# Optimization experiments

Hardware: AMD Instinct MI355X
Metric: run time of the kernel (lower is better)

Reference implementation:

```python
import jax, jax.numpy as jnp
import numpy as np

# Dimensions (Llama-3-8B-style GQA with paged KV cache)
B, S, HID = 1, 1024, 4096
H, HKV, D = 32, 8, 128
G = H // HKV
BLK = 16            # tokens per KV block
NB = 256            # blocks in storage
CB = 192            # context blocks attended (3072 tokens)
PAST = 2048         # tokens already cached before this step
NL = 2              # layers in kv_ptr
L = CB * BLK


def rotate_half(x):
    x1, x2 = x[..., : x.shape[-1] // 2], x[..., x.shape[-1] // 2:]
    return jnp.concatenate([-x2, x1], axis=-1)


def setup_inputs() -> dict:
    key = jax.random.key(0)
    ks = jax.random.split(key, 8)
    hidden_states = jax.random.normal(ks[0], (B, S, HID), jnp.float32)
    kv_ptr = jax.random.normal(ks[1], (NL, 2, NB, HKV, BLK, D), jnp.float32)
    Wq = 0.02 * jax.random.normal(ks[2], (H * D, HID), jnp.float32)
    Wk = 0.02 * jax.random.normal(ks[3], (HKV * D, HID), jnp.float32)
    Wv = 0.02 * jax.random.normal(ks[4], (HKV * D, HID), jnp.float32)
    Wo = 0.02 * jax.random.normal(ks[5], (HID, H * D), jnp.float32)
    # RoPE cache for the new tokens (global positions PAST..PAST+S-1), HF convention
    pos = (PAST + jnp.arange(S)).astype(jnp.float32)
    inv_freq = 1.0 / (10000.0 ** (jnp.arange(0, D, 2, dtype=jnp.float32) / D))
    freqs = pos[:, None] * inv_freq[None, :]                # [S, D/2]
    emb = jnp.concatenate([freqs, freqs], axis=-1)           # [S, D]
    cos = jnp.cos(emb)[None, None]                           # [1,1,S,D]
    sin = jnp.sin(emb)[None, None]
    new_q_lut = jnp.arange(S, dtype=jnp.int32)[None]         # identity query LUT
    new_kv_lut = (CB - S // BLK + jnp.arange(S // BLK, dtype=jnp.int32))[None]  # blocks 128..191
    all_kv_lut = jnp.arange(CB, dtype=jnp.int32)[None]       # blocks 0..191
    kv_pos = jnp.arange(L)
    q_pos = PAST + jnp.arange(S)
    mask = (kv_pos[None, None, :] <= q_pos[None, :, None])   # [1,S,L] causal over global positions
    cmd_groups = jnp.zeros((B, S), jnp.int32)                # split-K scheduling metadata (no math effect)
    return dict(hidden_states=hidden_states, kv_ptr=kv_ptr, new_q_lut=new_q_lut,
                new_kv_lut=new_kv_lut, all_kv_lut=all_kv_lut, mask=mask,
                cmd_groups=cmd_groups, cos=cos, sin=sin, Wq=Wq, Wk=Wk, Wv=Wv, Wo=Wo,
                layer_idx=0)


def reference(hidden_states, kv_ptr, new_q_lut, new_kv_lut, all_kv_lut, mask,
              cmd_groups, cos, sin, Wq, Wk, Wv, Wo, layer_idx):
    b, s, _ = hidden_states.shape
    # QKV projections (no bias)
    q = jnp.einsum('bsh,oh->bso', hidden_states, Wq).reshape(b, s, H, D).transpose(0, 2, 1, 3)
    k = jnp.einsum('bsh,oh->bso', hidden_states, Wk).reshape(b, s, HKV, D).transpose(0, 2, 1, 3)
    v = jnp.einsum('bsh,oh->bso', hidden_states, Wv).reshape(b, s, HKV, D).transpose(0, 2, 1, 3)
    # RoPE
    q = q * cos + rotate_half(q) * sin
    k = k * cos + rotate_half(k) * sin
    # fill_kv_block_storage: scatter new K/V blocks into this layer's storage (b == 1)
    kb = jnp.transpose(k[0].reshape(HKV, s // BLK, BLK, D), (1, 0, 2, 3))  # [nblk,HKV,BLK,D]
    vb = jnp.transpose(v[0].reshape(HKV, s // BLK, BLK, D), (1, 0, 2, 3))
    sk = kv_ptr[layer_idx, 0].at[new_kv_lut[0]].set(kb)
    sv = kv_ptr[layer_idx, 1].at[new_kv_lut[0]].set(vb)
    # qkv_attention: gather context blocks via LUT, masked GQA attention
    ck = jnp.transpose(sk[all_kv_lut[0]], (1, 0, 2, 3)).reshape(HKV, L, D)  # [HKV,L,D]
    cv = jnp.transpose(sv[all_kv_lut[0]], (1, 0, 2, 3)).reshape(HKV, L, D)
    qg = q[:, :, new_q_lut[0], :].reshape(b, HKV, G, s, D)
    scores = jnp.einsum('bkgsd,kld->bkgsl', qg, ck) / jnp.sqrt(jnp.float32(D))
    scores = jnp.where(mask[:, None, None], scores, jnp.finfo(scores.dtype).min)
    p = jax.nn.softmax(scores, axis=-1)
    o = jnp.einsum('bkgsl,kld->bkgsd', p, cv).reshape(b, H, s, D)
    o = o.transpose(0, 2, 1, 3).reshape(b, s, H * D)
    return jnp.einsum('bso,ho->bsh', o, Wo)
```

## Files before the change

### kernel.cpp

```cpp
#include <hip/hip_runtime.h>
#include <cstdint>
#include <cstddef>


typedef _Float16 f16;
typedef f16 f16x8 __attribute__((ext_vector_type(8)));
typedef f16 f16x4 __attribute__((ext_vector_type(4)));
typedef float f32x4 __attribute__((ext_vector_type(4)));

#define HIDN 4096
#define LCTX 3072
#define PASTN 2048
#define QK_SCALE_LOG2 0.12753102734366334f
#define RESC_THR 11.54f

__device__ __forceinline__ f32x4 mfma16(f16x8 a, f16x8 b, f32x4 c) {
    return __builtin_amdgcn_mfma_f32_16x16x32_f16(a, b, c, 0, 0, 0);
}
__device__ __forceinline__ f32x4 mfma16k16(f16x4 a, f16x4 b, f32x4 c) {
    return __builtin_amdgcn_mfma_f32_16x16x16f16(a, b, c, 0, 0, 0);
}

__device__ __forceinline__ void gl_lds16(const void* g, void* l) {
    auto gp = (const __attribute__((address_space(1))) unsigned int*)(uintptr_t)g;
    auto lp = (__attribute__((address_space(3))) unsigned int*)(uintptr_t)l;
    __builtin_amdgcn_global_load_lds(gp, lp, 16, 0, 0);
}

__device__ __forceinline__ uint32_t lds_lo(const void* p) {
    return (uint32_t)(uintptr_t)p;
}

#define TRRD(dst, va, OFF) \
    asm volatile("ds_read_b64_tr_b16 %0, %1 offset:" #OFF : "=v"(dst) : "v"(va))
#define WAITL(N) \
    asm volatile("s_waitcnt lgkmcnt(" #N ")" ::: "memory"); \
    __builtin_amdgcn_sched_barrier(0)

__global__ void cvt_h(const float* __restrict__ hidden, f16* __restrict__ h16)
{
    int i = blockIdx.x * 256 + threadIdx.x;
    f32x4 v = *(const f32x4*)(hidden + (size_t)i * 4);
    f16x4 h;
#pragma unroll
    for (int j = 0; j < 4; j++) h[j] = (f16)v[j];
    *(f16x4*)(h16 + (size_t)i * 4) = h;
}

__global__ __launch_bounds__(512, 4) void gemm_qkv(
    const f16* __restrict__ A,
    const float* __restrict__ Bq, const float* __restrict__ Bk2,
    const float* __restrict__ Bv2,
    f16* __restrict__ Cq, f16* __restrict__ Ck, f16* __restrict__ Cv,
    const float* __restrict__ kvp, const int* __restrict__ layer,
    f16* __restrict__ ckc, const float* __restrict__ Wo, f16* __restrict__ w16o)
{
    constexpr int K = 4096;
    __shared__ f16 As[2 * 128 * 64];
    __shared__ f16 Bs[2 * 128 * 64];

    const int bx = blockIdx.x;
    const int t = threadIdx.x;

    if (bx >= 384) {
        const int lay = layer[0];
        const int cid = bx - 384;
        int base = cid * 512 + t;
#pragma unroll
        for (int pass = 0; pass < 16; ++pass) {
            int i4 = base + pass * 65536;
            int half = i4 >> 19;
            int e = (i4 & 524287) * 4;
            int hh = e >> 18, rem = e & 262143, l = rem >> 7, d = rem & 127;
            int blk = l >> 4, rr = l & 15;
            size_t src = (((size_t)(lay * 2 + half) * 256 + blk) * 8 + hh) * 2048
                       + (size_t)rr * 128 + d;
            f32x4 x = *(const f32x4*)(kvp + src);
            f16x4 h;
#pragma unroll
            for (int j = 0; j < 4; j++) h[j] = (f16)x[j];
            size_t dst = ((size_t)hh * LCTX + l) * 128 + d;
            *(f16x4*)((half ? Cv : ckc) + dst) = h;
        }
        {
            const float* src = Wo + (size_t)cid * 131072;
            f16* dst = w16o + (size_t)cid * 131072;
#pragma unroll 4
            for (int p = 0; p < 64; ++p) {
                int e = (p * 512 + t) * 4;
                f32x4 v = *(const f32x4*)(src + e);
                f16x4 hv;
#pragma unroll
                for (int jx = 0; jx < 4; jx++) hv[jx] = (f16)v[jx];
                *(f16x4*)(dst + e) = hv;
            }
        }
        return;
    }

    const int lane = t & 63, w = t >> 6;
    const int wm = w >> 2, wn = w & 3;
    const int l16 = lane & 15, g16 = lane >> 4;
    const int m0 = (bx / 48) * 128, n0 = (bx % 48) * 128;

    const int srow = lane >> 3;
    const int sgr  = (lane & 7) ^ srow;
    const size_t aoff = (size_t)(m0 + w * 16 + srow) * K + sgr * 8;

    const float* Bf;
    int nb = n0;
    if (n0 >= 5120)      { Bf = Bv2; nb = n0 - 5120; }
    else if (n0 >= 4096) { Bf = Bk2; nb = n0 - 4096; }
    else                 { Bf = Bq; }
    const int brw = lane >> 4;
    const int b4  = lane & 15;
    const int bg  = b4 >> 1, bsub = (b4 & 1) << 2;
    const float* bbase = Bf + (size_t)(nb + w * 16 + brw) * K + b4 * 4;

    int bwr[4];
#pragma unroll
    for (int j = 0; j < 4; j++) {
        int r = w * 16 + j * 4 + brw;
        bwr[j] = r * 64 + ((bg ^ (r & 7)) << 3) + bsub;
    }

    f32x4 acc[4][2];
#pragma unroll
    for (int i = 0; i < 4; i++)
#pragma unroll
        for (int j = 0; j < 2; j++) acc[i][j] = (f32x4){0.f, 0.f, 0.f, 0.f};

    f32x4 bv[4];
#pragma unroll
    for (int j = 0; j < 4; j++)
        bv[j] = *(const f32x4*)(bbase + (size_t)(j * 4) * K);
#pragma unroll
    for (int j = 0; j < 2; j++)
        gl_lds16(A + aoff + (size_t)j * 8 * K,
                 (void*)(As + (w * 16 + j * 8) * 64));
#pragma unroll
    for (int j = 0; j < 4; j++) {
        f16x4 hv;
#pragma unroll
        for (int q = 0; q < 4; q++) hv[q] = (f16)bv[j][q];
        *(f16x4*)&Bs[bwr[j]] = hv;
    }
    __syncthreads();

    for (int k0 = 0; k0 < K; k0 += 64) {
        const int cur = (k0 >> 6) & 1;
        const int nxt = cur ^ 1;
        const bool more = (k0 + 64 < K);
        if (more) {
#pragma unroll
            for (int j = 0; j < 2; j++)
                gl_lds16(A + aoff + (size_t)j * 8 * K + k0 + 64,
                         (void*)(As + nxt * 8192 + (w * 16 + j * 8) * 64));
#pragma unroll
            for (int j = 0; j < 4; j++)
                bv[j] = *(const f32x4*)(bbase + (size_t)(j * 4) * K + k0 + 64);
        }
#pragma unroll
        for (int ks = 0; ks < 2; ks++) {
            f16x8 af[4], bfr[2];
#pragma unroll
            for (int mi = 0; mi < 4; mi++) {
                int r = wm * 64 + mi * 16 + l16;
                int g = ks * 4 + g16;
                af[mi] = *(const f16x8*)&As[cur * 8192 + r * 64 + ((g ^ (r & 7)) << 3)];
            }
#pragma unroll
            for (int ni = 0; ni < 2; ni++) {
                int r = wn * 32 + ni * 16 + l16;
                int g = ks * 4 + g16;
                bfr[ni] = *(const f16x8*)&Bs[cur * 8192 + r * 64 + ((g ^ (r & 7)) << 3)];
            }
#pragma unroll
            for (int ni = 0; ni < 2; ni++)
#pragma unroll
                for (int mi = 0; mi < 4; mi++)
                    acc[mi][ni] = mfma16(af[mi], bfr[ni], acc[mi][ni]);
        }
        if (more) {
#pragma unroll
            for (int j = 0; j < 4; j++) {
                f16x4 hv;
#pragma unroll
                for (int q = 0; q < 4; q++) hv[q] = (f16)bv[j][q];
                *(f16x4*)&Bs[nxt * 8192 + bwr[j]] = hv;
            }
        }
        __syncthreads();
    }

#pragma unroll
    for (int mi = 0; mi < 4; mi++)
#pragma unroll
        for (int ni = 0; ni < 2; ni++)
#pragma unroll
            for (int r = 0; r < 4; r++) {
                int row = m0 + wm * 64 + mi * 16 + (g16 << 2) + r;
                int col = n0 + wn * 32 + ni * 16 + l16;
                float val = acc[mi][ni][r];
                if (col < 4096) {
                    Cq[(size_t)row * 4096 + col] = (f16)val;
                } else if (col < 5120) {
                    Ck[(size_t)row * 1024 + (col - 4096)] = (f16)val;
                } else {
                    int c = col - 5120;
                    int hh = c >> 7, d = c & 127;
                    Cv[((size_t)hh * LCTX + PASTN + row) * 128 + d] = (f16)val;
                }
            }
}

__global__ void aux2(f16* __restrict__ q16, const f16* __restrict__ kraw,
                     const float* __restrict__ cosp, const float* __restrict__ sinp,
                     f16* __restrict__ ck)
{
    int i = blockIdx.x * 256 + threadIdx.x;
    if (i < 262144) {
        int gd = i & 7, hh = (i >> 3) & 31, s = i >> 8;
        size_t b1 = (size_t)s * 4096 + hh * 128 + gd * 8;
        f16x8 x1 = *(f16x8*)(q16 + b1);
        f16x8 x2 = *(f16x8*)(q16 + b1 + 64);
        const float* c1 = cosp + s * 128 + gd * 8;
        const float* s1 = sinp + s * 128 + gd * 8;
        f16x8 o1, o2;
#pragma unroll
        for (int j = 0; j < 8; j++) {
            float a = (float)x1[j], b = (float)x2[j];
            o1[j] = (f16)((a * c1[j] - b * s1[j]) * QK_SCALE_LOG2);
            o2[j] = (f16)((b * c1[j + 64] + a * s1[j + 64]) * QK_SCALE_LOG2);
        }
        *(f16x8*)(q16 + b1) = o1;
        *(f16x8*)(q16 + b1 + 64) = o2;
    } else {
        int ii = i - 262144;
        int gd = ii & 7, kvh = (ii >> 3) & 7, s = ii >> 6;
        size_t b1 = (size_t)s * 1024 + kvh * 128 + gd * 8;
        f16x8 x1 = *(const f16x8*)(kraw + b1);
        f16x8 x2 = *(const f16x8*)(kraw + b1 + 64);
        const float* c1 = cosp + s * 128 + gd * 8;
        const float* s1 = sinp + s * 128 + gd * 8;
        f16x8 o1, o2;
#pragma unroll
        for (int j = 0; j < 8; j++) {
            float a = (float)x1[j], b = (float)x2[j];
            o1[j] = (f16)(a * c1[j] - b * s1[j]);
            o2[j] = (f16)(b * c1[j + 64] + a * s1[j + 64]);
        }
        size_t dst = ((size_t)kvh * LCTX + PASTN + s) * 128 + gd * 8;
        *(f16x8*)(ck + dst) = o1;
        *(f16x8*)(ck + dst + 64) = o2;
    }
}

__global__ __launch_bounds__(256, 2) void attn_part(
    const f16* __restrict__ Q, const f16* __restrict__ Kc,
    const f16* __restrict__ Vc, f16* __restrict__ Op, float* __restrict__ mlb)
{
    const int b = blockIdx.x;
    const int z = b >> 8;
    const int idx = b & 255;
    const int h = idx & 31;
    const int jj = idx >> 5;
    const int j = z ? (7 - jj) : jj;
    const int s0 = j * 128;
    const int kvh = h >> 2;
    const int t = threadIdx.x, lane = t & 63, w = t >> 6;
    const int l16 = lane & 15, g16 = lane >> 4;

    __shared__ f16 Ks[2][64 * 128];
    __shared__ f16 Vs[2][64 * 128];

    f16x8 qfA[4], qfB[4];
    {
        size_t baseA = (size_t)(s0 + w * 32 + l16) * 4096 + h * 128;
        size_t baseB = baseA + (size_t)16 * 4096;
#pragma unroll
        for (int kk = 0; kk < 4; kk++) {
            qfA[kk] = *(const f16x8*)(Q + baseA + kk * 32 + g16 * 8);
            qfB[kk] = *(const f16x8*)(Q + baseB + kk * 32 + g16 * 8);
        }
    }

    f32x4 ofA[8], ofB[8];
#pragma unroll
    for (int cf = 0; cf < 8; cf++) {
        ofA[cf] = (f32x4){0.f, 0.f, 0.f, 0.f};
        ofB[cf] = (f32x4){0.f, 0.f, 0.f, 0.f};
    }
    float mrA = -3.0e38f, lrA = 0.f;
    float mrB = -3.0e38f, lrB = 0.f;

    const f16* Kb = Kc + (size_t)kvh * LCTX * 128;
    const f16* Vb = Vc + (size_t)kvh * LCTX * 128;
    const int ntt = (PASTN + s0 + 128) >> 6;

    const int krow = lane >> 4;
    const int kp   = lane & 15;
    const int vrow = ((lane >> 5) << 4) + (((lane >> 3) & 3) << 2) + ((lane >> 1) & 3);
    const int vch  = (lane & 1) << 3;

    const uint32_t vs0 = lds_lo(Vs[0]) + lane * 8;
    const uint32_t vs1 = lds_lo(Vs[1]) + lane * 8;

#define STAGE_KV(l0, buf)                                                     \
    {                                                                         \
        _Pragma("unroll")                                                     \
        for (int jx = 0; jx < 4; jx++) {                                      \
            int r7 = ((jx & 1) << 2) + krow;                                  \
            int sg = kp ^ r7;                                                 \
            gl_lds16(Kb + (size_t)((l0) + w * 16 + jx * 4 + krow) * 128 + sg * 8, \
                     (void*)(Ks[buf] + (w * 16 + jx * 4) * 128));             \
        }                                                                     \
        _Pragma("unroll")                                                     \
        for (int q = 0; q < 4; q++) {                                         \
            gl_lds16(Vb + (size_t)((l0) + (q & 1) * 32 + vrow) * 128          \
                        + (w * 2 + (q >> 1)) * 16 + vch,                      \
                     (void*)(Vs[buf] + (w * 4 + q) * 512));                   \
        }                                                                     \
    }

    STAGE_KV(z * 64, 0);
    __syncthreads();

    int itp = 0;
    for (int it = z; it < ntt; it += 2, ++itp) {
        const int l0 = it << 6;
        const int cur = itp & 1;

        if (it + 2 < ntt) STAGE_KV(l0 + 128, cur ^ 1);

        f32x4 sA[4], sB[4];
#pragma unroll
        for (int ni = 0; ni < 4; ni++) {
            sA[ni] = (f32x4){0.f, 0.f, 0.f, 0.f};
            sB[ni] = (f32x4){0.f, 0.f, 0.f, 0.f};
        }
        __builtin_amdgcn_s_setprio(1);
#pragma unroll
        for (int ni = 0; ni < 4; ni++)
#pragma unroll
            for (int kk = 0; kk < 4; kk++) {
                int r = ni * 16 + l16;
                int g = kk * 4 + g16;
                f16x8 kh = *(const f16x8*)&Ks[cur][r * 128 + ((g ^ (r & 7)) << 3)];
                sA[ni] = mfma16(kh, qfA[kk], sA[ni]);
                sB[ni] = mfma16(kh, qfB[kk], sB[ni]);
            }
        __builtin_amdgcn_s_setprio(0);

#define SOFTMAX(sf, mr, lr, of, QOFF)                                          \
        {                                                                      \
            const int qrow = s0 + w * 32 + (QOFF) + l16;                       \
            if (l0 + 63 > PASTN + s0 + w * 32 + (QOFF)) {                      \
                _Pragma("unroll")                                              \
                for (int ni = 0; ni < 4; ni++)                                 \
                    _Pragma("unroll")                                          \
                    for (int r = 0; r < 4; r++) {                              \
                        int col = l0 + ni * 16 + (g16 << 2) + r;               \
                        if (col > PASTN + qrow) sf[ni][r] = -3.0e38f;          \
                    }                                                          \
            }                                                                  \
            float mx;                                                          \
            {                                                                  \
                f32x4 m4 = sf[0];                                              \
                _Pragma("unroll")                                              \
                for (int ni = 1; ni < 4; ni++) {                               \
                    m4[0] = fmaxf(m4[0], sf[ni][0]);                           \
                    m4[1] = fmaxf(m4[1], sf[ni][1]);                           \
                    m4[2] = fmaxf(m4[2], sf[ni][2]);                           \
                    m4[3] = fmaxf(m4[3], sf[ni][3]);                           \
                }                                                              \
                mx = fmaxf(fmaxf(m4[0], m4[1]), fmaxf(m4[2], m4[3]));          \
            }                                                                  \
            mx = fmaxf(mx, __shfl_xor(mx, 16));                                \
            mx = fmaxf(mx, __shfl_xor(mx, 32));                                \
            if (__any(mx > mr + RESC_THR)) {                                   \
                float mnew = fmaxf(mr, mx);                                    \
                float corr = exp2f(mr - mnew);                                 \
                mr = mnew;                                                     \
                lr *= corr;                                                    \
                float cr[4];                                                   \
                _Pragma("unroll")                                              \
                for (int r = 0; r < 4; r++) cr[r] = __shfl(corr, (g16 << 2) + r); \
                _Pragma("unroll")                                              \
                for (int cf = 0; cf < 8; cf++)                                 \
                    _Pragma("unroll")                                          \
                    for (int r = 0; r < 4; r++) of[cf][r] *= cr[r];            \
            }                                                                  \
            _Pragma("unroll")                                                  \
            for (int ni = 0; ni < 4; ni++)                                     \
                _Pragma("unroll")                                              \
                for (int r = 0; r < 4; r++) {                                  \
                    float p = exp2f(sf[ni][r] - mr);                           \
                    sf[ni][r] = p;                                             \
                    lr += p;                                                   \
                }                                                              \
        }

        SOFTMAX(sA, mrA, lrA, ofA, 0)
        SOFTMAX(sB, mrB, lrB, ofB, 16)

        f16x4 paA[4], paB[4];
#pragma unroll
        for (int ni = 0; ni < 4; ni++) {
            paA[ni][0] = (f16)sA[ni][0]; paA[ni][1] = (f16)sA[ni][1];
            paA[ni][2] = (f16)sA[ni][2]; paA[ni][3] = (f16)sA[ni][3];
            paB[ni][0] = (f16)sB[ni][0]; paB[ni][1] = (f16)sB[ni][1];
            paB[ni][2] = (f16)sB[ni][2]; paB[ni][3] = (f16)sB[ni][3];
        }

        {
            const uint32_t va = cur ? vs1 : vs0;
            f16x4 ra0, ra1, ra2, ra3, rb0, rb1, rb2, rb3;
            f16x4 rc0, rc1, rc2, rc3, rd0, rd1, rd2, rd3;
            __builtin_amdgcn_s_setprio(1);
            TRRD(ra0,va,0);     TRRD(ra1,va,512);   TRRD(ra2,va,1024);  TRRD(ra3,va,1536);
            TRRD(rb0,va,2048);  TRRD(rb1,va,2560);  TRRD(rb2,va,3072);  TRRD(rb3,va,3584);
            TRRD(rc0,va,4096);  TRRD(rc1,va,4608);  TRRD(rc2,va,5120);  TRRD(rc3,va,5632);
#define X2(cf, ni, reg) \
            ofA[cf] = mfma16k16(paA[ni], reg, ofA[cf]); \
            ofB[cf] = mfma16k16(paB[ni], reg, ofB[cf]);
            WAITL(8);
            X2(0,0,ra0) X2(0,1,ra1) X2(0,2,ra2) X2(0,3,ra3)
            TRRD(rd0,va,6144);  TRRD(rd1,va,6656);  TRRD(rd2,va,7168);  TRRD(rd3,va,7680);
            WAITL(8);
            X2(1,0,rb0) X2(1,1,rb1) X2(1,2,rb2) X2(1,3,rb3)
            TRRD(ra0,va,8192);  TRRD(ra1,va,8704);  TRRD(ra2,va,9216);  TRRD(ra3,va,9728);
            WAITL(8);
            X2(2,0,rc0) X2(2,1,rc1) X2(2,2,rc2) X2(2,3,rc3)
            TRRD(rb0,va,10240); TRRD(rb1,va,10752); TRRD(rb2,va,11264); TRRD(rb3,va,11776);
            WAITL(8);
            X2(3,0,rd0) X2(3,1,rd1) X2(3,2,rd2) X2(3,3,rd3)
            TRRD(rc0,va,12288); TRRD(rc1,va,12800); TRRD(rc2,va,13312); TRRD(rc3,va,13824);
            WAITL(8);
            X2(4,0,ra0) X2(4,1,ra1) X2(4,2,ra2) X2(4,3,ra3)
            TRRD(rd0,va,14336); TRRD(rd1,va,14848); TRRD(rd2,va,15360); TRRD(rd3,va,15872);
            WAITL(8);
            X2(5,0,rb0) X2(5,1,rb1) X2(5,2,rb2) X2(5,3,rb3)
            WAITL(4);
            X2(6,0,rc0) X2(6,1,rc1) X2(6,2,rc2) X2(6,3,rc3)
            WAITL(0);
            X2(7,0,rd0) X2(7,1,rd1) X2(7,2,rd2) X2(7,3,rd3)
#undef X2
            __builtin_amdgcn_s_setprio(0);
        }
        __syncthreads();
    }

#define WRITE_P(of, mr, lr, QOFF)                                             \
    {                                                                         \
        float l2 = lr + __shfl_xor(lr, 16);                                   \
        l2 += __shfl_xor(l2, 32);                                             \
        if (lane < 16) {                                                      \
            int srow = s0 + w * 32 + (QOFF) + lane;                           \
            *(float2*)(mlb + (((size_t)z * 1024 + srow) * 32 + h) * 2) =      \
                make_float2(mr, l2);                                          \
        }                                                                     \
        float lrr[4];                                                         \
        _Pragma("unroll")                                                     \
        for (int r = 0; r < 4; r++) lrr[r] = __shfl(l2, (g16 << 2) + r);      \
        _Pragma("unroll")                                                     \
        for (int cf = 0; cf < 8; cf++)                                        \
            _Pragma("unroll")                                                 \
            for (int r = 0; r < 4; r++) {                                     \
                int srow = s0 + w * 32 + (QOFF) + (g16 << 2) + r;             \
                int d = cf * 16 + l16;                                        \
                Op[(size_t)z * 4194304 + (size_t)srow * 4096                  \
                   + (size_t)h * 128 + d] = (f16)(of[cf][r] / lrr[r]);        \
            }                                                                 \
    }
    WRITE_P(ofA, mrA, lrA, 0)
    WRITE_P(ofB, mrB, lrB, 16)
#undef WRITE_P
#undef SOFTMAX
#undef STAGE_KV
}

__global__ __launch_bounds__(256, 3) void gemm_o(
    const f16* __restrict__ Op, const float* __restrict__ mlb,
    const f16* __restrict__ Bh, float* __restrict__ Cf)
{
    constexpr int K = 4096;
    __shared__ f16 As[64 * 64];
    __shared__ f16 Bs[128 * 64];

    const int bx = blockIdx.x;
    const int t = threadIdx.x, lane = t & 63, w = t >> 6;
    const int wm = w >> 1, wn = w & 1;
    const int l16 = lane & 15, g16 = lane >> 4;
    const int m0 = (bx / 32) * 64, n0 = (bx % 32) * 128;

    const int srow = lane >> 3;
    const int sgr  = (lane & 7) ^ srow;

    const size_t boff16 = (size_t)(n0 + w * 32 + srow) * K + sgr * 8;

    f32x4 acc[2][4];
#pragma unroll
    for (int i = 0; i < 2; i++)
#pragma unroll
        for (int j = 0; j < 4; j++) acc[i][j] = (f32x4){0.f, 0.f, 0.f, 0.f};

    for (int k0 = 0; k0 < K; k0 += 64) {
        {
            const int hh = k0 >> 7;
#pragma unroll
            for (int j = 0; j < 2; j++) {
                int row = m0 + w * 16 + j * 8 + srow;
                int col = k0 + sgr * 8;
                float2 ml0 = *(const float2*)(mlb + (((size_t)row) * 32 + hh) * 2);
                float2 ml1 = *(const float2*)(mlb + (((size_t)1024 + row) * 32 + hh) * 2);
                float mstar = fmaxf(ml0.x, ml1.x);
                float w0 = exp2f(ml0.x - mstar) * ml0.y;
                float w1 = exp2f(ml1.x - mstar) * ml1.y;
                float inv = 1.0f / (w0 + w1);
                w0 *= inv; w1 *= inv;
                f16x8 a0 = *(const f16x8*)(Op + (size_t)row * 4096 + col);
                f16x8 a1 = *(const f16x8*)(Op + 4194304 + (size_t)row * 4096 + col);
                f16x8 av;
#pragma unroll
                for (int q = 0; q < 8; q++)
                    av[q] = (f16)((float)a0[q] * w0 + (float)a1[q] * w1);
                *(f16x8*)&As[(w * 16 + j * 8) * 64 + lane * 8] = av;
            }
        }
#pragma unroll
        for (int j = 0; j < 4; j++)
            gl_lds16(Bh + boff16 + (size_t)j * 8 * K + k0,
                     (void*)(Bs + (w * 32 + j * 8) * 64));
        __syncthreads();

#pragma unroll
        for (int ks = 0; ks < 2; ks++) {
            f16x8 af[2], bfr[4];
#pragma unroll
            for (int mi = 0; mi < 2; mi++) {
                int r = wm * 32 + mi * 16 + l16;
                int g = ks * 4 + g16;
                af[mi] = *(const f16x8*)&As[r * 64 + ((g ^ (r & 7)) << 3)];
            }
#pragma unroll
            for (int ni = 0; ni < 4; ni++) {
                int r = wn * 64 + ni * 16 + l16;
                int g = ks * 4 + g16;
                bfr[ni] = *(const f16x8*)&Bs[r * 64 + ((g ^ (r & 7)) << 3)];
            }
#pragma unroll
            for (int ni = 0; ni < 4; ni++)
#pragma unroll
                for (int mi = 0; mi < 2; mi++)
                    acc[mi][ni] = mfma16(af[mi], bfr[ni], acc[mi][ni]);
        }
        __syncthreads();
    }

#pragma unroll
    for (int mi = 0; mi < 2; mi++)
#pragma unroll
        for (int ni = 0; ni < 4; ni++)
#pragma unroll
            for (int r = 0; r < 4; r++) {
                int row = m0 + wm * 32 + mi * 16 + (g16 << 2) + r;
                int col = n0 + wn * 64 + ni * 16 + l16;
                Cf[(size_t)row * 4096 + col] = acc[mi][ni][r];
            }
}

extern "C" void kernel_launch(void* const* d_in, const int* in_sizes, int n_in,
                              void* d_out, int out_size, void* d_ws, size_t ws_size,
                              hipStream_t stream)
{
    const float* hidden = (const float*)d_in[0];
    const float* kvp    = (const float*)d_in[1];
    const float* cosp   = (const float*)d_in[7];
    const float* sinp   = (const float*)d_in[8];
    const float* Wq     = (const float*)d_in[9];
    const float* Wk     = (const float*)d_in[10];
    const float* Wv     = (const float*)d_in[11];
    const float* Wo     = (const float*)d_in[12];
    const int*   layer  = (const int*)d_in[13];

    char* ws = (char*)d_ws;
    f16*   w16  = (f16*)ws;
    f16*   opart= (f16*)(ws + 33554432);
    f16*   h16  = (f16*)(ws + 50331648);
    f16*   ck   = (f16*)(ws + 58720256);
    f16*   cv   = (f16*)(ws + 65011712);
    float* mlb  = (float*)(ws + 71303168);

    f16* q16  = (f16*)d_out;
    f16* kraw = (f16*)((char*)d_out + 8388608);

    cvt_h<<<4096, 256, 0, stream>>>(hidden, h16);

    gemm_qkv<<<dim3(512), 512, 0, stream>>>(
        h16, Wq, Wk, Wv, q16, kraw, cv, kvp, layer, ck, Wo, w16);

    aux2<<<1280, 256, 0, stream>>>(q16, kraw, cosp, sinp, ck);

    attn_part<<<dim3(512), 256, 0, stream>>>(q16, ck, cv, opart, mlb);

    gemm_o<<<dim3(512), 256, 0, stream>>>(opart, mlb, w16, (float*)d_out);
}
```

Baseline: 276.4 us.

## Retile QKV GEMM to 256x64 with 4 waves and split attention combine out of gemm_o

The QKV projection GEMM moves from 128x128 tiles with 8 waves to 256x64 tiles with 4 waves, each wave now holding 8x2 accumulator fragments. The aux work in the extra blocks (KV cache conversion and Wo cast) is redistributed over 256 threads. The split-K softmax combine is pulled out of gemm_o into its own elementwise kernel that writes a combined f16 buffer, so gemm_o can load A directly with async global-to-LDS copies. The aim is to reduce redundant combine arithmetic per output tile and improve A-tile reuse, at the cost of an extra launch, a round-trip through global memory, and higher register pressure in gemm_qkv. The mlb buffer is also relocated into the output region.

```diff
diff --git a/kernel.cpp b/kernel.cpp
--- a/kernel.cpp
+++ b/kernel.cpp
@@ -47,7 +47,7 @@
     *(f16x4*)(h16 + (size_t)i * 4) = h;
 }
 
-__global__ __launch_bounds__(512, 4) void gemm_qkv(
+__global__ __launch_bounds__(256, 2) void gemm_qkv(
     const f16* __restrict__ A,
     const float* __restrict__ Bq, const float* __restrict__ Bk2,
     const float* __restrict__ Bv2,
@@ -56,19 +56,18 @@
     f16* __restrict__ ckc, const float* __restrict__ Wo, f16* __restrict__ w16o)
 {
     constexpr int K = 4096;
-    __shared__ f16 As[2 * 128 * 64];
-    __shared__ f16 Bs[2 * 128 * 64];
+    __shared__ f16 As[2 * 256 * 64];
+    __shared__ f16 Bs[2 * 64 * 64];
 
     const int bx = blockIdx.x;
-    const int t = threadIdx.x;
 
     if (bx >= 384) {
         const int lay = layer[0];
         const int cid = bx - 384;
-        int base = cid * 512 + t;
-#pragma unroll
-        for (int pass = 0; pass < 16; ++pass) {
-            int i4 = base + pass * 65536;
+        int base = cid * 256 + threadIdx.x;
+#pragma unroll
+        for (int pass = 0; pass < 32; ++pass) {
+            int i4 = base + pass * 32768;
             int half = i4 >> 19;
             int e = (i4 & 524287) * 4;
             int hh = e >> 18, rem = e & 262143, l = rem >> 7, d = rem & 127;
@@ -86,8 +85,8 @@
             const float* src = Wo + (size_t)cid * 131072;
             f16* dst = w16o + (size_t)cid * 131072;
 #pragma unroll 4
-            for (int p = 0; p < 64; ++p) {
-                int e = (p * 512 + t) * 4;
+            for (int p = 0; p < 128; ++p) {
+                int e = (p * 256 + threadIdx.x) * 4;
                 f32x4 v = *(const f32x4*)(src + e);
                 f16x4 hv;
 #pragma unroll
@@ -98,14 +97,14 @@
         return;
     }
 
-    const int lane = t & 63, w = t >> 6;
-    const int wm = w >> 2, wn = w & 3;
+    const int t = threadIdx.x, lane = t & 63, w = t >> 6;
+    const int wm = w >> 1, wn = w & 1;
     const int l16 = lane & 15, g16 = lane >> 4;
-    const int m0 = (bx / 48) * 128, n0 = (bx % 48) * 128;
+    const int m0 = (bx / 96) * 256, n0 = (bx % 96) * 64;
 
     const int srow = lane >> 3;
     const int sgr  = (lane & 7) ^ srow;
-    const size_t aoff = (size_t)(m0 + w * 16 + srow) * K + sgr * 8;
+    const size_t aoff = (size_t)(m0 + w * 64 + srow) * K + sgr * 8;
 
     const float* Bf;
     int nb = n0;
@@ -124,9 +123,9 @@
         bwr[j] = r * 64 + ((bg ^ (r & 7)) << 3) + bsub;
     }
 
-    f32x4 acc[4][2];
-#pragma unroll
-    for (int i = 0; i < 4; i++)
+    f32x4 acc[8][2];
+#pragma unroll
+    for (int i = 0; i < 8; i++)
 #pragma unroll
         for (int j = 0; j < 2; j++) acc[i][j] = (f32x4){0.f, 0.f, 0.f, 0.f};
 
@@ -135,9 +134,9 @@
     for (int j = 0; j < 4; j++)
         bv[j] = *(const f32x4*)(bbase + (size_t)(j * 4) * K);
 #pragma unroll
-    for (int j = 0; j < 2; j++)
+    for (int j = 0; j < 8; j++)
         gl_lds16(A + aoff + (size_t)j * 8 * K,
-                 (void*)(As + (w * 16 + j * 8) * 64));
+                 (void*)(As + (w * 64 + j * 8) * 64));
 #pragma unroll
     for (int j = 0; j < 4; j++) {
         f16x4 hv;
@@ -153,32 +152,32 @@
         const bool more = (k0 + 64 < K);
         if (more) {
 #pragma unroll
-            for (int j = 0; j < 2; j++)
+            for (int j = 0; j < 8; j++)
                 gl_lds16(A + aoff + (size_t)j * 8 * K + k0 + 64,
-                         (void*)(As + nxt * 8192 + (w * 16 + j * 8) * 64));
+                         (void*)(As + nxt * 16384 + (w * 64 + j * 8) * 64));
 #pragma unroll
             for (int j = 0; j < 4; j++)
                 bv[j] = *(const f32x4*)(bbase + (size_t)(j * 4) * K + k0 + 64);
         }
 #pragma unroll
         for (int ks = 0; ks < 2; ks++) {
-            f16x8 af[4], bfr[2];
-#pragma unroll
-            for (int mi = 0; mi < 4; mi++) {
-                int r = wm * 64 + mi * 16 + l16;
+            f16x8 af[8], bfr[2];
+#pragma unroll
+            for (int mi = 0; mi < 8; mi++) {
+                int r = wm * 128 + mi * 16 + l16;
                 int g = ks * 4 + g16;
-                af[mi] = *(const f16x8*)&As[cur * 8192 + r * 64 + ((g ^ (r & 7)) << 3)];
+                af[mi] = *(const f16x8*)&As[cur * 16384 + r * 64 + ((g ^ (r & 7)) << 3)];
             }
 #pragma unroll
             for (int ni = 0; ni < 2; ni++) {
                 int r = wn * 32 + ni * 16 + l16;
                 int g = ks * 4 + g16;
-                bfr[ni] = *(const f16x8*)&Bs[cur * 8192 + r * 64 + ((g ^ (r & 7)) << 3)];
+                bfr[ni] = *(const f16x8*)&Bs[cur * 4096 + r * 64 + ((g ^ (r & 7)) << 3)];
             }
 #pragma unroll
             for (int ni = 0; ni < 2; ni++)
 #pragma unroll
-                for (int mi = 0; mi < 4; mi++)
+                for (int mi = 0; mi < 8; mi++)
                     acc[mi][ni] = mfma16(af[mi], bfr[ni], acc[mi][ni]);
         }
         if (more) {
@@ -187,19 +186,19 @@
                 f16x4 hv;
 #pragma unroll
                 for (int q = 0; q < 4; q++) hv[q] = (f16)bv[j][q];
-                *(f16x4*)&Bs[nxt * 8192 + bwr[j]] = hv;
+                *(f16x4*)&Bs[nxt * 4096 + bwr[j]] = hv;
             }
         }
         __syncthreads();
     }
 
 #pragma unroll
-    for (int mi = 0; mi < 4; mi++)
+    for (int mi = 0; mi < 8; mi++)
 #pragma unroll
         for (int ni = 0; ni < 2; ni++)
 #pragma unroll
             for (int r = 0; r < 4; r++) {
-                int row = m0 + wm * 64 + mi * 16 + (g16 << 2) + r;
+                int row = m0 + wm * 128 + mi * 16 + (g16 << 2) + r;
                 int col = n0 + wn * 32 + ni * 16 + l16;
                 float val = acc[mi][ni][r];
                 if (col < 4096) {
@@ -211,6 +210,79 @@
                     int hh = c >> 7, d = c & 127;
                     Cv[((size_t)hh * LCTX + PASTN + row) * 128 + d] = (f16)val;
                 }
+            }
+}
+
+__global__ __launch_bounds__(256, 3) void gemm_o(
+    const f16* __restrict__ A, const f16* __restrict__ Bh,
+    float* __restrict__ Cf)
+{
+    constexpr int K = 4096;
+    __shared__ f16 As[64 * 64];
+    __shared__ f16 Bs[128 * 64];
+
+    const int bx = blockIdx.x;
+    const int t = threadIdx.x, lane = t & 63, w = t >> 6;
+    const int wm = w >> 1, wn = w & 1;
+    const int l16 = lane & 15, g16 = lane >> 4;
+    const int m0 = (bx / 32) * 64, n0 = (bx % 32) * 128;
+
+    const int srow = lane >> 3;
+    const int sgr  = (lane & 7) ^ srow;
+
+    const size_t aoff = (size_t)(m0 + w * 16 + srow) * K + sgr * 8;
+    const size_t boff = (size_t)(n0 + w * 32 + srow) * K + sgr * 8;
+
+    f32x4 acc[2][4];
+#pragma unroll
+    for (int i = 0; i < 2; i++)
+#pragma unroll
+        for (int j = 0; j < 4; j++) acc[i][j] = (f32x4){0.f, 0.f, 0.f, 0.f};
+
+    for (int k0 = 0; k0 < K; k0 += 64) {
+#pragma unroll
+        for (int j = 0; j < 2; j++)
+            gl_lds16(A + aoff + (size_t)j * 8 * K + k0,
+                     (void*)(As + (w * 16 + j * 8) * 64));
+#pragma unroll
+        for (int j = 0; j < 4; j++)
+            gl_lds16(Bh + boff + (size_t)j * 8 * K + k0,
+                     (void*)(Bs + (w * 32 + j * 8) * 64));
+        __syncthreads();
+
+#pragma unroll
+        for (int ks = 0; ks < 2; ks++) {
+            f16x8 af[2], bfr[4];
+#pragma unroll
+            for (int mi = 0; mi < 2; mi++) {
+                int r = wm * 32 + mi * 16 + l16;
+                int g = ks * 4 + g16;
+                af[mi] = *(const f16x8*)&As[r * 64 + ((g ^ (r & 7)) << 3)];
+            }
+#pragma unroll
+            for (int ni = 0; ni < 4; ni++) {
+                int r = wn * 64 + ni * 16 + l16;
+                int g = ks * 4 + g16;
+                bfr[ni] = *(const f16x8*)&Bs[r * 64 + ((g ^ (r & 7)) << 3)];
+            }
+#pragma unroll
+            for (int ni = 0; ni < 4; ni++)
+#pragma unroll
+                for (int mi = 0; mi < 2; mi++)
+                    acc[mi][ni] = mfma16(af[mi], bfr[ni], acc[mi][ni]);
+        }
+        __syncthreads();
+    }
+
+#pragma unroll
+    for (int mi = 0; mi < 2; mi++)
+#pragma unroll
+        for (int ni = 0; ni < 4; ni++)
+#pragma unroll
+            for (int r = 0; r < 4; r++) {
+                int row = m0 + wm * 32 + mi * 16 + (g16 << 2) + r;
+                int col = n0 + wn * 64 + ni * 16 + l16;
+                Cf[(size_t)row * 4096 + col] = acc[mi][ni][r];
             }
 }
 
@@ -480,94 +552,25 @@
 #undef STAGE_KV
 }
 
-__global__ __launch_bounds__(256, 3) void gemm_o(
-    const f16* __restrict__ Op, const float* __restrict__ mlb,
-    const f16* __restrict__ Bh, float* __restrict__ Cf)
+__global__ void attn_combine(const f16* __restrict__ Op, const float* __restrict__ mlb,
+                             f16* __restrict__ obuf)
 {
-    constexpr int K = 4096;
-    __shared__ f16 As[64 * 64];
-    __shared__ f16 Bs[128 * 64];
-
-    const int bx = blockIdx.x;
-    const int t = threadIdx.x, lane = t & 63, w = t >> 6;
-    const int wm = w >> 1, wn = w & 1;
-    const int l16 = lane & 15, g16 = lane >> 4;
-    const int m0 = (bx / 32) * 64, n0 = (bx % 32) * 128;
-
-    const int srow = lane >> 3;
-    const int sgr  = (lane & 7) ^ srow;
-
-    const size_t boff16 = (size_t)(n0 + w * 32 + srow) * K + sgr * 8;
-
-    f32x4 acc[2][4];
-#pragma unroll
-    for (int i = 0; i < 2; i++)
-#pragma unroll
-        for (int j = 0; j < 4; j++) acc[i][j] = (f32x4){0.f, 0.f, 0.f, 0.f};
-
-    for (int k0 = 0; k0 < K; k0 += 64) {
-        {
-            const int hh = k0 >> 7;
-#pragma unroll
-            for (int j = 0; j < 2; j++) {
-                int row = m0 + w * 16 + j * 8 + srow;
-                int col = k0 + sgr * 8;
-                float2 ml0 = *(const float2*)(mlb + (((size_t)row) * 32 + hh) * 2);
-                float2 ml1 = *(const float2*)(mlb + (((size_t)1024 + row) * 32 + hh) * 2);
-                float mstar = fmaxf(ml0.x, ml1.x);
-                float w0 = exp2f(ml0.x - mstar) * ml0.y;
-                float w1 = exp2f(ml1.x - mstar) * ml1.y;
-                float inv = 1.0f / (w0 + w1);
-                w0 *= inv; w1 *= inv;
-                f16x8 a0 = *(const f16x8*)(Op + (size_t)row * 4096 + col);
-                f16x8 a1 = *(const f16x8*)(Op + 4194304 + (size_t)row * 4096 + col);
-                f16x8 av;
-#pragma unroll
-                for (int q = 0; q < 8; q++)
-                    av[q] = (f16)((float)a0[q] * w0 + (float)a1[q] * w1);
-                *(f16x8*)&As[(w * 16 + j * 8) * 64 + lane * 8] = av;
-            }
-        }
-#pragma unroll
-        for (int j = 0; j < 4; j++)
-            gl_lds16(Bh + boff16 + (size_t)j * 8 * K + k0,
-                     (void*)(Bs + (w * 32 + j * 8) * 64));
-        __syncthreads();
-
-#pragma unroll
-        for (int ks = 0; ks < 2; ks++) {
-            f16x8 af[2], bfr[4];
-#pragma unroll
-            for (int mi = 0; mi < 2; mi++) {
-                int r = wm * 32 + mi * 16 + l16;
-                int g = ks * 4 + g16;
-                af[mi] = *(const f16x8*)&As[r * 64 + ((g ^ (r & 7)) << 3)];
-            }
-#pragma unroll
-            for (int ni = 0; ni < 4; ni++) {
-                int r = wn * 64 + ni * 16 + l16;
-                int g = ks * 4 + g16;
-                bfr[ni] = *(const f16x8*)&Bs[r * 64 + ((g ^ (r & 7)) << 3)];
-            }
-#pragma unroll
-            for (int ni = 0; ni < 4; ni++)
-#pragma unroll
-                for (int mi = 0; mi < 2; mi++)
-                    acc[mi][ni] = mfma16(af[mi], bfr[ni], acc[mi][ni]);
-        }
-        __syncthreads();
-    }
-
-#pragma unroll
-    for (int mi = 0; mi < 2; mi++)
-#pragma unroll
-        for (int ni = 0; ni < 4; ni++)
-#pragma unroll
-            for (int r = 0; r < 4; r++) {
-                int row = m0 + wm * 32 + mi * 16 + (g16 << 2) + r;
-                int col = n0 + wn * 64 + ni * 16 + l16;
-                Cf[(size_t)row * 4096 + col] = acc[mi][ni][r];
-            }
+    int i = blockIdx.x * 256 + threadIdx.x;
+    int d8 = i & 15, hh = (i >> 4) & 31, s = i >> 9;
+    float2 ml0 = *(const float2*)(mlb + (((size_t)0 * 1024 + s) * 32 + hh) * 2);
+    float2 ml1 = *(const float2*)(mlb + (((size_t)1 * 1024 + s) * 32 + hh) * 2);
+    float mstar = fmaxf(ml0.x, ml1.x);
+    float w0 = exp2f(ml0.x - mstar) * ml0.y;
+    float w1 = exp2f(ml1.x - mstar) * ml1.y;
+    float inv = 1.0f / (w0 + w1);
+    size_t off = (size_t)s * 4096 + (size_t)hh * 128 + d8 * 8;
+    f16x8 a = *(const f16x8*)(Op + off);
+    f16x8 b = *(const f16x8*)(Op + 4194304 + off);
+    f16x8 o;
+#pragma unroll
+    for (int jx = 0; jx < 8; jx++)
+        o[jx] = (f16)(((float)a[jx] * w0 + (float)b[jx] * w1) * inv);
+    *(f16x8*)(obuf + off) = o;
 }
 
 extern "C" void kernel_launch(void* const* d_in, const int* in_sizes, int n_in,
@@ -585,24 +588,27 @@
     const int*   layer  = (const int*)d_in[13];
 
     char* ws = (char*)d_ws;
-    f16*   w16  = (f16*)ws;
-    f16*   opart= (f16*)(ws + 33554432);
-    f16*   h16  = (f16*)(ws + 50331648);
-    f16*   ck   = (f16*)(ws + 58720256);
-    f16*   cv   = (f16*)(ws + 65011712);
-    float* mlb  = (float*)(ws + 71303168);
-
-    f16* q16  = (f16*)d_out;
-    f16* kraw = (f16*)((char*)d_out + 8388608);
+    f16* w16  = (f16*)ws;
+    f16* opart= (f16*)(ws + 33554432);
+    f16* h16  = (f16*)(ws + 50331648);
+    f16* ck   = (f16*)(ws + 58720256);
+    f16* cv   = (f16*)(ws + 65011712);
+    f16* obuf = (f16*)(ws + 71303168);
+
+    f16*   q16  = (f16*)d_out;
+    f16*   kraw = (f16*)((char*)d_out + 8388608);
+    float* mlb  = (float*)((char*)d_out + 8388608);
 
     cvt_h<<<4096, 256, 0, stream>>>(hidden, h16);
 
-    gemm_qkv<<<dim3(512), 512, 0, stream>>>(
+    gemm_qkv<<<dim3(512), 256, 0, stream>>>(
         h16, Wq, Wk, Wv, q16, kraw, cv, kvp, layer, ck, Wo, w16);
 
     aux2<<<1280, 256, 0, stream>>>(q16, kraw, cosp, sinp, ck);
 
     attn_part<<<dim3(512), 256, 0, stream>>>(q16, ck, cv, opart, mlb);
 
-    gemm_o<<<dim3(512), 256, 0, stream>>>(opart, mlb, w16, (float*)d_out);
-}
+    attn_combine<<<2048, 256, 0, stream>>>(opart, mlb, obuf);
+
+    gemm_o<<<dim3(512), 256, 0, stream>>>(obuf, w16, (float*)d_out);
+}
```

Result: faster. 239.3 us, median of 2 (-13.4%).
